# Kernel tuning notes

Measured on AMD Instinct MI355X. Metric: run time of the kernel, lower is better.

The kernel has to match this reference:

```python
import jax, jax.numpy as jnp
import numpy as np
from jax import lax

N, D, H, E = 8192, 1024, 4096, 8


def setup_inputs() -> dict:
    key = jax.random.key(0)
    ks = jax.random.split(key, 7)
    s = 0.02
    return {
        "x": jax.random.normal(ks[0], (N, D), dtype=jnp.float32),
        "Wr": jax.random.normal(ks[1], (E, D), dtype=jnp.float32) * s,
        "br": jnp.zeros((E,), dtype=jnp.float32),
        "Wup": jax.random.normal(ks[2], (E, H, D), dtype=jnp.float32) * s,
        "bup": jnp.zeros((E, H), dtype=jnp.float32),
        "Wdown": jax.random.normal(ks[3], (E, D, H), dtype=jnp.float32) * s,
        "bdown": jnp.zeros((E, D), dtype=jnp.float32),
    }


def reference(x, Wr, br, Wup, bup, Wdown, bdown):
    # Router: softmax over logits; only argmax is used (softmax is monotone,
    # argmax of softmax == argmax of logits).
    logits = x @ Wr.T + br            # [N, E]
    scores = jax.nn.softmax(logits, axis=-1)
    top1 = jnp.argmax(scores, axis=-1)  # [N] int

    out0 = jnp.zeros_like(x)

    def body(out, ew):
        i, Wu, bu, Wd, bd = ew
        h = jax.nn.silu(x @ Wu.T + bu)   # [N, H]
        y = h @ Wd.T + bd                # [N, D]
        out = jnp.where((top1 == i)[:, None], y, out)
        return out, None

    idx = jnp.arange(Wup.shape[0])
    out, _ = lax.scan(body, out0, (idx, Wup, bup, Wdown, bdown))
    return out
```

## Files before the change

### kernel.cpp

```cpp
#include <hip/hip_runtime.h>

#define NT 8192
#define DD 1024
#define HH 4096
#define EE 8

typedef __attribute__((ext_vector_type(8))) short short8;
typedef __attribute__((ext_vector_type(4))) float f32x4;

__device__ __forceinline__ unsigned short f2bf(float f) {
    unsigned int u = __float_as_uint(f);
    u += 0x7FFFu + ((u >> 16) & 1u);
    return (unsigned short)(u >> 16);
}

__device__ __forceinline__ void gload_lds16(const void* g, void* l) {
    __builtin_amdgcn_global_load_lds(
        (const __attribute__((address_space(1))) unsigned int*)g,
        (__attribute__((address_space(3))) unsigned int*)l, 16, 0, 0);
}

__global__ __launch_bounds__(256) void cvtw_kernel(const float* __restrict__ a,
                                                   const float* __restrict__ b,
                                                   unsigned short* __restrict__ da,
                                                   unsigned short* __restrict__ db) {
    const size_t half = (size_t)EE * HH * DD;
    size_t i = ((size_t)blockIdx.x * 256 + threadIdx.x) * 8;
    const float* s; unsigned short* d;
    if (i < half) { s = a + i; d = da + i; }
    else          { s = b + (i - half); d = db + (i - half); }
    float4 v0 = ((const float4*)s)[0];
    float4 v1 = ((const float4*)s)[1];
    ushort4 o0, o1;
    o0.x = f2bf(v0.x); o0.y = f2bf(v0.y); o0.z = f2bf(v0.z); o0.w = f2bf(v0.w);
    o1.x = f2bf(v1.x); o1.y = f2bf(v1.y); o1.z = f2bf(v1.z); o1.w = f2bf(v1.w);
    ((ushort4*)d)[0] = o0;
    ((ushort4*)d)[1] = o1;
}

__global__ __launch_bounds__(256) void router_kernel(const float* __restrict__ x,
                                                     const float* __restrict__ Wr,
                                                     const float* __restrict__ br,
                                                     int* __restrict__ counts,
                                                     int* __restrict__ tlist) {
    __shared__ float sW[EE * DD];
    const int t = threadIdx.x;
    for (int i = t; i < EE * DD / 4; i += 256)
        ((float4*)sW)[i] = ((const float4*)Wr)[i];
    __syncthreads();
    const int lane = t & 63;
    const int wv = t >> 6;
    const int token = blockIdx.x * 4 + wv;
    const float* xr = x + (size_t)token * DD;
    float acc[EE];
#pragma unroll
    for (int e = 0; e < EE; e++) acc[e] = 0.f;
    for (int k = lane; k < DD; k += 64) {
        float xv = xr[k];
#pragma unroll
        for (int e = 0; e < EE; e++) acc[e] += xv * sW[e * DD + k];
    }
#pragma unroll
    for (int off = 32; off > 0; off >>= 1) {
#pragma unroll
        for (int e = 0; e < EE; e++) acc[e] += __shfl_xor(acc[e], off);
    }
    if (lane == 0) {
        int best = 0;
        float bv = acc[0] + br[0];
#pragma unroll
        for (int e = 1; e < EE; e++) {
            float v = acc[e] + br[e];
            if (v > bv) { bv = v; best = e; }
        }
        int pos = atomicAdd(&counts[best], 1);
        tlist[best * NT + pos] = token;
    }
}

__global__ __launch_bounds__(256) void gather_kernel(const float* __restrict__ x,
                                                     const int* __restrict__ tlist,
                                                     const int* __restrict__ counts,
                                                     unsigned short* __restrict__ xg) {
    const int row = blockIdx.x * 4 + (threadIdx.x >> 6);
    const int lane = threadIdx.x & 63;
    int off[EE];
    int s = 0;
#pragma unroll
    for (int k = 0; k < EE; k++) { off[k] = s; s += counts[k]; }
    int e = 0;
#pragma unroll
    for (int k = 1; k < EE; k++)
        if (row >= off[k]) e = k;
    const int token = tlist[e * NT + row - off[e]];
    const float4* src = (const float4*)(x + (size_t)token * DD);
    ushort4* dst = (ushort4*)(xg + (size_t)row * DD);
#pragma unroll
    for (int it = 0; it < 4; it++) {
        float4 v = src[it * 64 + lane];
        ushort4 o;
        o.x = f2bf(v.x); o.y = f2bf(v.y); o.z = f2bf(v.z); o.w = f2bf(v.w);
        dst[it * 64 + lane] = o;
    }
}


#define SLOTS 72

struct SlotDec { int e, off_e, cnt, m0, ok; };

__device__ __forceinline__ SlotDec decode_slot(const int* __restrict__ counts, int slot) {
    SlotDec d; d.ok = 0; d.e = 0; d.off_e = 0; d.cnt = 0; d.m0 = 0;
    int s = 0, csum = 0;
#pragma unroll
    for (int k = 0; k < EE; k++) {
        int ck = counts[k];
        int mb = (ck + 127) >> 7;
        if (!d.ok && slot < csum + mb) {
            d.ok = 1; d.e = k; d.off_e = s; d.cnt = ck; d.m0 = (slot - csum) * 128;
        }
        s += ck; csum += mb;
    }
    return d;
}

__global__ __launch_bounds__(256) void up_gemm(const unsigned short* __restrict__ xg,
                                               const unsigned short* __restrict__ Wub,
                                               const float* __restrict__ bup,
                                               const int* __restrict__ counts,
                                               unsigned short* __restrict__ hbuf) {
    SlotDec sd = decode_slot(counts, blockIdx.y);
    if (!sd.ok) return;
    const int e = sd.e, off_e = sd.off_e, cnt = sd.cnt, m0 = sd.m0;
    const int n0 = blockIdx.x * 128;
    const int t = threadIdx.x;

    __shared__ unsigned short sA[2][128 * 32];
    __shared__ unsigned short sB[2][128 * 32];

    const int r0 = t >> 2;
    const int kc = (t & 3) ^ ((r0 >> 1) & 3);
    const int c1 = cnt - 1;
    int ra = m0 + r0;      if (ra > c1) ra = c1;
    int rb = m0 + 64 + r0; if (rb > c1) rb = c1;
    const unsigned short* gA0 = xg + (size_t)(off_e + ra) * DD + kc * 8;
    const unsigned short* gA1 = xg + (size_t)(off_e + rb) * DD + kc * 8;
    const unsigned short* gB0 = Wub + ((size_t)e * HH + n0 + r0) * DD + kc * 8;
    const unsigned short* gB1 = Wub + ((size_t)e * HH + n0 + 64 + r0) * DD + kc * 8;

    const int lane = t & 63;
    const int wm = ((t >> 6) & 1) * 64;
    const int wn = (t >> 7) * 64;
    const int mrow = lane & 15;
    const int kq = lane >> 4;
    const int slot = (kq ^ ((mrow >> 1) & 3)) * 8;

    f32x4 acc[4][4];
#pragma unroll
    for (int i = 0; i < 4; i++)
#pragma unroll
        for (int j = 0; j < 4; j++)
            acc[i][j] = (f32x4){0.f, 0.f, 0.f, 0.f};

    auto STAGE = [&](int buf, int kt) {
        gload_lds16(gA0 + kt, &sA[buf][t * 8]);
        gload_lds16(gA1 + kt, &sA[buf][(t + 256) * 8]);
        gload_lds16(gB0 + kt, &sB[buf][t * 8]);
        gload_lds16(gB1 + kt, &sB[buf][(t + 256) * 8]);
    };

    STAGE(0, 0);
    int cur = 0;
    for (int kt = 0; kt < DD; kt += 32) {
        __syncthreads();
        if (kt + 32 < DD) STAGE(cur ^ 1, kt + 32);
        short8 a[4], b[4];
#pragma unroll
        for (int i = 0; i < 4; i++) {
            a[i] = *(const short8*)(&sA[cur][(wm + i * 16 + mrow) * 32 + slot]);
            b[i] = *(const short8*)(&sB[cur][(wn + i * 16 + mrow) * 32 + slot]);
        }
#pragma unroll
        for (int i = 0; i < 4; i++)
#pragma unroll
            for (int j = 0; j < 4; j++)
                acc[i][j] = __builtin_amdgcn_mfma_f32_16x16x32_bf16(a[i], b[j], acc[i][j], 0, 0, 0);
        cur ^= 1;
    }

    float bias[4];
#pragma unroll
    for (int j = 0; j < 4; j++) bias[j] = bup[e * HH + n0 + wn + j * 16 + mrow];
#pragma unroll
    for (int i = 0; i < 4; i++) {
#pragma unroll
        for (int r = 0; r < 4; r++) {
            int m = m0 + wm + i * 16 + kq * 4 + r;
            if (m < cnt) {
                unsigned short* hrow = hbuf + (size_t)(off_e + m) * HH + n0 + wn + mrow;
#pragma unroll
                for (int j = 0; j < 4; j++) {
                    float v = acc[i][j][r] + bias[j];
                    v = v / (1.f + __expf(-v));
                    hrow[j * 16] = f2bf(v);
                }
            }
        }
    }
}

__global__ __launch_bounds__(256) void down_gemm(const unsigned short* __restrict__ hbuf,
                                                 const unsigned short* __restrict__ Wdb,
                                                 const float* __restrict__ bdown,
                                                 const int* __restrict__ counts,
                                                 const int* __restrict__ tlist,
                                                 float* __restrict__ out) {
    const int lin = blockIdx.x;
    const int rm = lin & 7;
    const int g  = lin >> 8;
    const int i_ = (lin >> 3) & 31;
    const int r  = g * 8 + rm;
    if (r >= (SLOTS / 4)) return;
    const int slot_id = r * 4 + (i_ & 3);
    const int nb = i_ >> 2;

    SlotDec sd = decode_slot(counts, slot_id);
    if (!sd.ok) return;
    const int e = sd.e, off_e = sd.off_e, cnt = sd.cnt, m0 = sd.m0;
    const int n0 = nb * 128;
    const int t = threadIdx.x;

    __shared__ unsigned short sA[2][128 * 32];
    __shared__ unsigned short sB[2][128 * 32];

    const int r0 = t >> 2;
    const int kc = (t & 3) ^ ((r0 >> 1) & 3);
    const int c1 = cnt - 1;
    int ra = m0 + r0;      if (ra > c1) ra = c1;
    int rb = m0 + 64 + r0; if (rb > c1) rb = c1;
    const unsigned short* gA0 = hbuf + (size_t)(off_e + ra) * HH + kc * 8;
    const unsigned short* gA1 = hbuf + (size_t)(off_e + rb) * HH + kc * 8;
    const unsigned short* gB0 = Wdb + ((size_t)e * DD + n0 + r0) * HH + kc * 8;
    const unsigned short* gB1 = Wdb + ((size_t)e * DD + n0 + 64 + r0) * HH + kc * 8;

    const int lane = t & 63;
    const int wm = ((t >> 6) & 1) * 64;
    const int wn = (t >> 7) * 64;
    const int mrow = lane & 15;
    const int kq = lane >> 4;
    const int slot = (kq ^ ((mrow >> 1) & 3)) * 8;

    f32x4 acc[4][4];
#pragma unroll
    for (int i = 0; i < 4; i++)
#pragma unroll
        for (int j = 0; j < 4; j++)
            acc[i][j] = (f32x4){0.f, 0.f, 0.f, 0.f};

    auto STAGE = [&](int buf, int kt) {
        gload_lds16(gA0 + kt, &sA[buf][t * 8]);
        gload_lds16(gA1 + kt, &sA[buf][(t + 256) * 8]);
        gload_lds16(gB0 + kt, &sB[buf][t * 8]);
        gload_lds16(gB1 + kt, &sB[buf][(t + 256) * 8]);
    };

    STAGE(0, 0);
    int cur = 0;
    for (int kt = 0; kt < HH; kt += 32) {
        __syncthreads();
        if (kt + 32 < HH) STAGE(cur ^ 1, kt + 32);
        short8 a[4], b[4];
#pragma unroll
        for (int i = 0; i < 4; i++) {
            a[i] = *(const short8*)(&sA[cur][(wm + i * 16 + mrow) * 32 + slot]);
            b[i] = *(const short8*)(&sB[cur][(wn + i * 16 + mrow) * 32 + slot]);
        }
#pragma unroll
        for (int i = 0; i < 4; i++)
#pragma unroll
            for (int j = 0; j < 4; j++)
                acc[i][j] = __builtin_amdgcn_mfma_f32_16x16x32_bf16(a[i], b[j], acc[i][j], 0, 0, 0);
        cur ^= 1;
    }

    const int* tl = tlist + e * NT;
    float bias[4];
#pragma unroll
    for (int j = 0; j < 4; j++) bias[j] = bdown[e * DD + n0 + wn + j * 16 + mrow];
#pragma unroll
    for (int i = 0; i < 4; i++) {
#pragma unroll
        for (int r2 = 0; r2 < 4; r2++) {
            int m = m0 + wm + i * 16 + kq * 4 + r2;
            if (m < cnt) {
                int token = tl[m];
                float* orow = out + (size_t)token * DD + n0 + wn + mrow;
#pragma unroll
                for (int j = 0; j < 4; j++)
                    orow[j * 16] = acc[i][j][r2] + bias[j];
            }
        }
    }
}

extern "C" void kernel_launch(void* const* d_in, const int* in_sizes, int n_in,
                              void* d_out, int out_size, void* d_ws, size_t ws_size,
                              hipStream_t stream) {
    const float* x     = (const float*)d_in[0];
    const float* Wr    = (const float*)d_in[1];
    const float* br    = (const float*)d_in[2];
    const float* Wup   = (const float*)d_in[3];
    const float* bup   = (const float*)d_in[4];
    const float* Wdown = (const float*)d_in[5];
    const float* bdown = (const float*)d_in[6];
    float* out = (float*)d_out;

    char* w = (char*)d_ws;
    int* counts  = (int*)w;               w += 256;
    int* tlist   = (int*)w;               w += (size_t)EE * NT * 4;
    unsigned short* xg   = (unsigned short*)w;  w += (size_t)NT * DD * 2;
    unsigned short* hbuf = (unsigned short*)w;  w += (size_t)NT * HH * 2;
    unsigned short* Wub  = (unsigned short*)w;  w += (size_t)EE * HH * DD * 2;
    unsigned short* Wdb  = (unsigned short*)w;

    hipMemsetAsync(counts, 0, EE * sizeof(int), stream);

    cvtw_kernel<<<(2 * (size_t)EE * HH * DD) / 2048, 256, 0, stream>>>(Wup, Wdown, Wub, Wdb);
    router_kernel<<<NT / 4, 256, 0, stream>>>(x, Wr, br, counts, tlist);
    gather_kernel<<<NT / 4, 256, 0, stream>>>(x, tlist, counts, xg);

    dim3 gu(HH / 128, SLOTS);
    up_gemm<<<gu, 256, 0, stream>>>(xg, Wub, bup, counts, hbuf);
    down_gemm<<<768, 256, 0, stream>>>(hbuf, Wdb, bdown, counts, tlist, out);
}
```

Measured before the change: 678.5 us.

## Fuse router with weight conversion and gather fp32 tokens directly in up GEMM

Merges the router and weight-conversion kernels into a single launch and drops the separate gather kernel. The up GEMM now reads fp32 activation rows through the token list, converts them to bf16 in registers and writes them to LDS itself. This removes the xg intermediate buffer and two launches. In exchange the A tile goes through register loads and LDS stores instead of direct global-to-LDS loads, and each A row is reread as fp32 by every N block, which roughly doubles the A-side traffic per block.

```diff
diff --git a/kernel.cpp b/kernel.cpp
--- a/kernel.cpp
+++ b/kernel.cpp
@@ -4,6 +4,7 @@
 #define DD 1024
 #define HH 4096
 #define EE 8
+#define RB (NT / 4)
 
 typedef __attribute__((ext_vector_type(8))) short short8;
 typedef __attribute__((ext_vector_type(4))) float f32x4;
@@ -14,93 +15,73 @@
     return (unsigned short)(u >> 16);
 }
 
+__device__ __forceinline__ short8 cvt8(float4 a, float4 b) {
+    short8 r;
+    r[0] = (short)f2bf(a.x); r[1] = (short)f2bf(a.y);
+    r[2] = (short)f2bf(a.z); r[3] = (short)f2bf(a.w);
+    r[4] = (short)f2bf(b.x); r[5] = (short)f2bf(b.y);
+    r[6] = (short)f2bf(b.z); r[7] = (short)f2bf(b.w);
+    return r;
+}
+
 __device__ __forceinline__ void gload_lds16(const void* g, void* l) {
     __builtin_amdgcn_global_load_lds(
         (const __attribute__((address_space(1))) unsigned int*)g,
         (__attribute__((address_space(3))) unsigned int*)l, 16, 0, 0);
 }
 
-__global__ __launch_bounds__(256) void cvtw_kernel(const float* __restrict__ a,
-                                                   const float* __restrict__ b,
-                                                   unsigned short* __restrict__ da,
-                                                   unsigned short* __restrict__ db) {
-    const size_t half = (size_t)EE * HH * DD;
-    size_t i = ((size_t)blockIdx.x * 256 + threadIdx.x) * 8;
-    const float* s; unsigned short* d;
-    if (i < half) { s = a + i; d = da + i; }
-    else          { s = b + (i - half); d = db + (i - half); }
-    float4 v0 = ((const float4*)s)[0];
-    float4 v1 = ((const float4*)s)[1];
-    ushort4 o0, o1;
-    o0.x = f2bf(v0.x); o0.y = f2bf(v0.y); o0.z = f2bf(v0.z); o0.w = f2bf(v0.w);
-    o1.x = f2bf(v1.x); o1.y = f2bf(v1.y); o1.z = f2bf(v1.z); o1.w = f2bf(v1.w);
-    ((ushort4*)d)[0] = o0;
-    ((ushort4*)d)[1] = o1;
-}
-
-__global__ __launch_bounds__(256) void router_kernel(const float* __restrict__ x,
-                                                     const float* __restrict__ Wr,
-                                                     const float* __restrict__ br,
-                                                     int* __restrict__ counts,
-                                                     int* __restrict__ tlist) {
+__global__ __launch_bounds__(256) void prep_kernel(const float* __restrict__ x,
+                                                   const float* __restrict__ Wr,
+                                                   const float* __restrict__ br,
+                                                   const float* __restrict__ Wup,
+                                                   const float* __restrict__ Wdown,
+                                                   int* __restrict__ counts,
+                                                   int* __restrict__ tlist,
+                                                   unsigned short* __restrict__ Wub,
+                                                   unsigned short* __restrict__ Wdb) {
     __shared__ float sW[EE * DD];
     const int t = threadIdx.x;
-    for (int i = t; i < EE * DD / 4; i += 256)
-        ((float4*)sW)[i] = ((const float4*)Wr)[i];
-    __syncthreads();
-    const int lane = t & 63;
-    const int wv = t >> 6;
-    const int token = blockIdx.x * 4 + wv;
-    const float* xr = x + (size_t)token * DD;
-    float acc[EE];
-#pragma unroll
-    for (int e = 0; e < EE; e++) acc[e] = 0.f;
-    for (int k = lane; k < DD; k += 64) {
-        float xv = xr[k];
-#pragma unroll
-        for (int e = 0; e < EE; e++) acc[e] += xv * sW[e * DD + k];
-    }
-#pragma unroll
-    for (int off = 32; off > 0; off >>= 1) {
-#pragma unroll
-        for (int e = 0; e < EE; e++) acc[e] += __shfl_xor(acc[e], off);
-    }
-    if (lane == 0) {
-        int best = 0;
-        float bv = acc[0] + br[0];
-#pragma unroll
-        for (int e = 1; e < EE; e++) {
-            float v = acc[e] + br[e];
-            if (v > bv) { bv = v; best = e; }
-        }
-        int pos = atomicAdd(&counts[best], 1);
-        tlist[best * NT + pos] = token;
-    }
-}
-
-__global__ __launch_bounds__(256) void gather_kernel(const float* __restrict__ x,
-                                                     const int* __restrict__ tlist,
-                                                     const int* __restrict__ counts,
-                                                     unsigned short* __restrict__ xg) {
-    const int row = blockIdx.x * 4 + (threadIdx.x >> 6);
-    const int lane = threadIdx.x & 63;
-    int off[EE];
-    int s = 0;
-#pragma unroll
-    for (int k = 0; k < EE; k++) { off[k] = s; s += counts[k]; }
-    int e = 0;
-#pragma unroll
-    for (int k = 1; k < EE; k++)
-        if (row >= off[k]) e = k;
-    const int token = tlist[e * NT + row - off[e]];
-    const float4* src = (const float4*)(x + (size_t)token * DD);
-    ushort4* dst = (ushort4*)(xg + (size_t)row * DD);
-#pragma unroll
-    for (int it = 0; it < 4; it++) {
-        float4 v = src[it * 64 + lane];
-        ushort4 o;
-        o.x = f2bf(v.x); o.y = f2bf(v.y); o.z = f2bf(v.z); o.w = f2bf(v.w);
-        dst[it * 64 + lane] = o;
+    if (blockIdx.x < RB) {
+        for (int i = t; i < EE * DD / 4; i += 256)
+            ((float4*)sW)[i] = ((const float4*)Wr)[i];
+        __syncthreads();
+        const int lane = t & 63;
+        const int wv = t >> 6;
+        const int token = blockIdx.x * 4 + wv;
+        const float* xr = x + (size_t)token * DD;
+        float acc[EE];
+#pragma unroll
+        for (int e = 0; e < EE; e++) acc[e] = 0.f;
+        for (int k = lane; k < DD; k += 64) {
+            float xv = xr[k];
+#pragma unroll
+            for (int e = 0; e < EE; e++) acc[e] += xv * sW[e * DD + k];
+        }
+#pragma unroll
+        for (int off = 32; off > 0; off >>= 1) {
+#pragma unroll
+            for (int e = 0; e < EE; e++) acc[e] += __shfl_xor(acc[e], off);
+        }
+        if (lane == 0) {
+            int best = 0;
+            float bv = acc[0] + br[0];
+#pragma unroll
+            for (int e = 1; e < EE; e++) {
+                float v = acc[e] + br[e];
+                if (v > bv) { bv = v; best = e; }
+            }
+            int pos = atomicAdd(&counts[best], 1);
+            tlist[best * NT + pos] = token;
+        }
+    } else {
+        const size_t half = (size_t)EE * HH * DD;
+        size_t i = ((size_t)(blockIdx.x - RB) * 256 + t) * 8;
+        const float* s; unsigned short* d;
+        if (i < half) { s = Wup + i; d = Wub + i; }
+        else          { s = Wdown + (i - half); d = Wdb + (i - half); }
+        float4 v0 = ((const float4*)s)[0];
+        float4 v1 = ((const float4*)s)[1];
+        *(short8*)d = cvt8(v0, v1);
     }
 }
 
@@ -124,7 +105,8 @@
     return d;
 }
 
-__global__ __launch_bounds__(256) void up_gemm(const unsigned short* __restrict__ xg,
+__global__ __launch_bounds__(256) void up_gemm(const float* __restrict__ x,
+                                               const int* __restrict__ tlist,
                                                const unsigned short* __restrict__ Wub,
                                                const float* __restrict__ bup,
                                                const int* __restrict__ counts,
@@ -143,8 +125,9 @@
     const int c1 = cnt - 1;
     int ra = m0 + r0;      if (ra > c1) ra = c1;
     int rb = m0 + 64 + r0; if (rb > c1) rb = c1;
-    const unsigned short* gA0 = xg + (size_t)(off_e + ra) * DD + kc * 8;
-    const unsigned short* gA1 = xg + (size_t)(off_e + rb) * DD + kc * 8;
+    const int* tl = tlist + e * NT;
+    const float* pA0 = x + (size_t)tl[ra] * DD + kc * 8;
+    const float* pA1 = x + (size_t)tl[rb] * DD + kc * 8;
     const unsigned short* gB0 = Wub + ((size_t)e * HH + n0 + r0) * DD + kc * 8;
     const unsigned short* gB1 = Wub + ((size_t)e * HH + n0 + 64 + r0) * DD + kc * 8;
 
@@ -162,18 +145,27 @@
         for (int j = 0; j < 4; j++)
             acc[i][j] = (f32x4){0.f, 0.f, 0.f, 0.f};
 
-    auto STAGE = [&](int buf, int kt) {
-        gload_lds16(gA0 + kt, &sA[buf][t * 8]);
-        gload_lds16(gA1 + kt, &sA[buf][(t + 256) * 8]);
+    float4 fa0, fa1, fa2, fa3;
+    auto ALOAD = [&](int kt) {
+        fa0 = *(const float4*)(pA0 + kt);
+        fa1 = *(const float4*)(pA0 + kt + 4);
+        fa2 = *(const float4*)(pA1 + kt);
+        fa3 = *(const float4*)(pA1 + kt + 4);
+    };
+    auto AWRITE = [&](int buf) {
+        *(short8*)&sA[buf][t * 8]         = cvt8(fa0, fa1);
+        *(short8*)&sA[buf][(t + 256) * 8] = cvt8(fa2, fa3);
+    };
+    auto BSTAGE = [&](int buf, int kt) {
         gload_lds16(gB0 + kt, &sB[buf][t * 8]);
         gload_lds16(gB1 + kt, &sB[buf][(t + 256) * 8]);
     };
 
-    STAGE(0, 0);
+    ALOAD(0); BSTAGE(0, 0); AWRITE(0);
     int cur = 0;
     for (int kt = 0; kt < DD; kt += 32) {
         __syncthreads();
-        if (kt + 32 < DD) STAGE(cur ^ 1, kt + 32);
+        if (kt + 32 < DD) { ALOAD(kt + 32); BSTAGE(cur ^ 1, kt + 32); }
         short8 a[4], b[4];
 #pragma unroll
         for (int i = 0; i < 4; i++) {
@@ -185,6 +177,7 @@
 #pragma unroll
             for (int j = 0; j < 4; j++)
                 acc[i][j] = __builtin_amdgcn_mfma_f32_16x16x32_bf16(a[i], b[j], acc[i][j], 0, 0, 0);
+        if (kt + 32 < DD) AWRITE(cur ^ 1);
         cur ^= 1;
     }
 
@@ -318,18 +311,16 @@
     char* w = (char*)d_ws;
     int* counts  = (int*)w;               w += 256;
     int* tlist   = (int*)w;               w += (size_t)EE * NT * 4;
-    unsigned short* xg   = (unsigned short*)w;  w += (size_t)NT * DD * 2;
     unsigned short* hbuf = (unsigned short*)w;  w += (size_t)NT * HH * 2;
     unsigned short* Wub  = (unsigned short*)w;  w += (size_t)EE * HH * DD * 2;
     unsigned short* Wdb  = (unsigned short*)w;
 
     hipMemsetAsync(counts, 0, EE * sizeof(int), stream);
 
-    cvtw_kernel<<<(2 * (size_t)EE * HH * DD) / 2048, 256, 0, stream>>>(Wup, Wdown, Wub, Wdb);
-    router_kernel<<<NT / 4, 256, 0, stream>>>(x, Wr, br, counts, tlist);
-    gather_kernel<<<NT / 4, 256, 0, stream>>>(x, tlist, counts, xg);
+    prep_kernel<<<RB + (2 * (size_t)EE * HH * DD) / 2048, 256, 0, stream>>>(
+        x, Wr, br, Wup, Wdown, counts, tlist, Wub, Wdb);
 
     dim3 gu(HH / 128, SLOTS);
-    up_gemm<<<gu, 256, 0, stream>>>(xg, Wub, bup, counts, hbuf);
+    up_gemm<<<gu, 256, 0, stream>>>(x, tlist, Wub, bup, counts, hbuf);
     down_gemm<<<768, 256, 0, stream>>>(hbuf, Wdb, bdown, counts, tlist, out);
 }
```

Result: slower. 765.0 us (+12.7%).
